# Optimization experiments

Measured on AMD Instinct MI355X. Metric: run time of the kernel, lower is better.

The kernel has to match this reference:

```python
import jax, jax.numpy as jnp
import numpy as np

B, C, H, W = 32, 384, 56, 56
SPARSE = 8
HEADS = 8
HIDDEN = 4 * C
EPS = 1e-5


def _ln(x, g, b):
    m = jnp.mean(x, axis=-1, keepdims=True)
    v = jnp.mean((x - m) ** 2, axis=-1, keepdims=True)
    return (x - m) * jax.lax.rsqrt(v + EPS) * g + b


def setup_inputs() -> dict:
    key = jax.random.key(0)
    ks = jax.random.split(key, 12)
    s = 0.02
    return {
        "x": jax.random.normal(ks[0], (B, C, H, W), jnp.float32),
        "ln1_g": jnp.ones((C,), jnp.float32),
        "ln1_b": jnp.zeros((C,), jnp.float32),
        "qkv_w": jax.random.normal(ks[1], (C, 3 * C), jnp.float32) * s,
        "proj_w": jax.random.normal(ks[2], (C, C), jnp.float32) * s,
        "proj_b": jnp.zeros((C,), jnp.float32),
        "ln2_g": jnp.ones((C,), jnp.float32),
        "ln2_b": jnp.zeros((C,), jnp.float32),
        "fc1_w": jax.random.normal(ks[3], (C, HIDDEN), jnp.float32) * s,
        "fc1_b": jnp.zeros((HIDDEN,), jnp.float32),
        "dw_w": jax.random.normal(ks[4], (HIDDEN, 1, 3, 3), jnp.float32) * np.sqrt(2.0 / 9.0),
        "dw_b": jnp.zeros((HIDDEN,), jnp.float32),
        "fc2_w": jax.random.normal(ks[5], (HIDDEN, C), jnp.float32) * s,
        "fc2_b": jnp.zeros((C,), jnp.float32),
        "gamma1": jnp.full((C,), 1e-6, jnp.float32),
        "gamma2": jnp.full((C,), 1e-6, jnp.float32),
    }


def reference(x, ln1_g, ln1_b, qkv_w, proj_w, proj_b, ln2_g, ln2_b,
              fc1_w, fc1_b, dw_w, dw_b, fc2_w, fc2_b, gamma1, gamma2):
    Bx, Cx, Hx, Wx = x.shape
    s = SPARSE
    g = Hx // s  # grid size; H divisible by sparse_size per module assert
    N = Hx * Wx
    hd = Cx // HEADS
    scale = hd ** (-0.5)

    x_before = x.reshape(Bx, Cx, N).transpose(0, 2, 1)  # [B,N,C]

    # alter_sparse: gather tokens spaced g apart into s x s windows
    xw = x.transpose(0, 2, 3, 1).reshape(Bx, s, g, s, g, Cx)
    xw = xw.transpose(0, 2, 4, 1, 3, 5).reshape(Bx * g * g, s * s, Cx)

    # attention on windows
    h = _ln(xw, ln1_g, ln1_b)
    qkv = (h @ qkv_w).reshape(Bx * g * g, s * s, 3, HEADS, hd)
    q, k, v = (qkv[:, :, i].transpose(0, 2, 1, 3) for i in range(3))  # [Bw,h,n,d]
    attn = jax.nn.softmax(jnp.einsum('bhqd,bhkd->bhqk', q, k) * scale, axis=-1)
    o = jnp.einsum('bhqk,bhkd->bhqd', attn, v).transpose(0, 2, 1, 3)
    o = o.reshape(Bx * g * g, s * s, Cx) @ proj_w + proj_b

    # alter_unsparse: scatter windows back to spatial layout
    o = o.reshape(Bx, g, g, s, s, Cx).transpose(0, 3, 1, 4, 2, 5)
    o = o.reshape(Bx, Hx, Wx, Cx).reshape(Bx, N, Cx)

    x1 = x_before + gamma1 * o

    # MLP with depthwise conv
    m = _ln(x1, ln2_g, ln2_b) @ fc1_w + fc1_b  # [B,N,hidden]
    m2 = m.transpose(0, 2, 1).reshape(Bx, HIDDEN, Hx, Wx)
    m2 = jax.lax.conv_general_dilated(
        m2, dw_w, window_strides=(1, 1), padding=((1, 1), (1, 1)),
        dimension_numbers=('NCHW', 'OIHW', 'NCHW'),
        feature_group_count=HIDDEN) + dw_b[None, :, None, None]
    m = m2.reshape(Bx, HIDDEN, N).transpose(0, 2, 1)
    m = jax.nn.gelu(m, approximate=False)
    m = m @ fc2_w + fc2_b

    x2 = x1 + gamma2 * m
    return x2.transpose(0, 2, 1).reshape(Bx, Cx, Hx, Wx)
```

## Files before the change

### kernel.cpp

```cpp
#include <hip/hip_runtime.h>
#include <hip/hip_bf16.h>

typedef __hip_bfloat16 bf16;
typedef float v4f __attribute__((ext_vector_type(4)));
typedef __attribute__((ext_vector_type(8))) short short8;

__device__ __forceinline__ float b2f(bf16 v) { return __bfloat162float(v); }
__device__ __forceinline__ bf16 f2b(float v) { return __float2bfloat16(v); }

__device__ __forceinline__ void gload_lds16(const bf16* g, bf16* l) {
    __builtin_amdgcn_global_load_lds((__attribute__((address_space(1))) void*)(void*)g,
                                     (__attribute__((address_space(3))) void*)l, 16, 0, 0);
}

#define BB 32
#define CD 384
#define HH 56
#define ND 3136
#define HID 1536
#define GG 7
#define SS 8
#define MROWS 100352

__device__ __forceinline__ int wrow_to_token(int orow) {
    int w = orow >> 6, t = orow & 63;
    int bb = w / 49, wr = w % 49;
    int gy = wr / GG, gx = wr % GG;
    int sy = t >> 3, sx = t & 7;
    return bb * ND + (sy * GG + gy) * HH + (sx * GG + gx);
}

__global__ __launch_bounds__(256) void transpose_f2b_k(const float* __restrict__ in,
                                                       bf16* __restrict__ out, int R, int Cc)
{
    __shared__ float tile[32][33];
    int c0 = blockIdx.x * 32, r0 = blockIdx.y * 32;
    size_t bb = blockIdx.z;
    int tx = threadIdx.x & 31, ty = threadIdx.x >> 5;
    const float* ip = in + bb * (size_t)R * Cc;
    bf16* op = out + bb * (size_t)R * Cc;
#pragma unroll
    for (int i = 0; i < 4; i++)
        tile[ty + i * 8][tx] = ip[(size_t)(r0 + ty + i * 8) * Cc + (c0 + tx)];
    __syncthreads();
#pragma unroll
    for (int i = 0; i < 4; i++)
        op[(size_t)(c0 + ty + i * 8) * R + (r0 + tx)] = f2b(tile[tx][ty + i * 8]);
}

__global__ __launch_bounds__(256) void ln_k(const bf16* __restrict__ in,
                                            const float* __restrict__ g,
                                            const float* __restrict__ b,
                                            bf16* __restrict__ out,
                                            int row0, int gather)
{
    int wave = threadIdx.x >> 6, lane = threadIdx.x & 63;
    int row = row0 + blockIdx.x * 4 + wave;
    int src = gather ? wrow_to_token(row) : row;
    const bf16* ip = in + (size_t)src * CD;
    float vals[6];
    float s = 0.f, s2 = 0.f;
#pragma unroll
    for (int i = 0; i < 6; i++) {
        float v = b2f(ip[lane + i * 64]);
        vals[i] = v; s += v; s2 += v * v;
    }
#pragma unroll
    for (int off = 32; off >= 1; off >>= 1) {
        s  += __shfl_xor(s, off);
        s2 += __shfl_xor(s2, off);
    }
    float mean = s * (1.f / CD);
    float var = s2 * (1.f / CD) - mean * mean;
    float rstd = rsqrtf(var + 1e-5f);
    bf16* op = out + (size_t)(row - row0) * CD;
#pragma unroll
    for (int i = 0; i < 6; i++) {
        int c = lane + i * 64;
        op[c] = f2b((vals[i] - mean) * rstd * g[c] + b[c]);
    }
}

__global__ __launch_bounds__(256) void gemm_bt(const bf16* __restrict__ A,
                                               const bf16* __restrict__ Bt,
                                               const float* __restrict__ bias,
                                               bf16* __restrict__ Cm,
                                               int M, int N, int K, int gx)
{
    __shared__ __align__(16) bf16 As[128][32];
    __shared__ __align__(16) bf16 Bs[128][32];
    const int nwg = gridDim.x;
    const int q = nwg >> 3, r = nwg & 7;
    const int xcd = blockIdx.x & 7, id8 = blockIdx.x >> 3;
    const int wgid = (xcd < r ? xcd * (q + 1) : r * (q + 1) + (xcd - r) * q) + id8;
    const int m0 = (wgid / gx) * 128, n0 = (wgid % gx) * 128;

    const int tid = threadIdx.x;
    const int lane = tid & 63, wave = tid >> 6;
    const int rb = (wave >> 1) * 64, cb = (wave & 1) * 64;
    const int lr = lane & 15, ko = (lane >> 4) * 8;
    const int srow = lane >> 2;
    const int scol = (lane & 3) * 8;

    v4f acc[4][4];
#pragma unroll
    for (int i = 0; i < 4; i++)
#pragma unroll
        for (int j = 0; j < 4; j++) acc[i][j] = (v4f)0.f;

    for (int kk = 0; kk < K; kk += 32) {
        const int r0 = wave * 32;
#pragma unroll
        for (int h = 0; h < 2; h++) {
            int row = r0 + h * 16 + srow;
            gload_lds16(&A [(size_t)(m0 + row) * K + kk + scol], &As[r0 + h * 16][0]);
            gload_lds16(&Bt[(size_t)(n0 + row) * K + kk + scol], &Bs[r0 + h * 16][0]);
        }
        __syncthreads();
        short8 af[4], bfr[4];
#pragma unroll
        for (int mi = 0; mi < 4; mi++) af[mi]  = *(const short8*)&As[rb + mi * 16 + lr][ko];
#pragma unroll
        for (int ni = 0; ni < 4; ni++) bfr[ni] = *(const short8*)&Bs[cb + ni * 16 + lr][ko];
#pragma unroll
        for (int mi = 0; mi < 4; mi++)
#pragma unroll
            for (int ni = 0; ni < 4; ni++)
                acc[mi][ni] = __builtin_amdgcn_mfma_f32_16x16x32_bf16(af[mi], bfr[ni], acc[mi][ni], 0, 0, 0);
        __syncthreads();
    }
#pragma unroll
    for (int ni = 0; ni < 4; ni++) {
        int col = n0 + cb + ni * 16 + lr;
        float bv = bias ? bias[col] : 0.f;
#pragma unroll
        for (int mi = 0; mi < 4; mi++) {
            int rowb = m0 + rb + mi * 16 + (lane >> 4) * 4;
#pragma unroll
            for (int r = 0; r < 4; r++)
                Cm[(size_t)(rowb + r) * N + col] = f2b(acc[mi][ni][r] + bv);
        }
    }
}

__global__ __launch_bounds__(64) void attn_mfma_k(const bf16* __restrict__ qkv,
                                                  bf16* __restrict__ o)
{
    __shared__ __align__(16) char lds[14336];
    char* Ps = lds;
    bf16* Vs = (bf16*)(lds + 8192);

    const int lane = threadIdx.x;
    const int lr = lane & 15, grp = lane >> 4;
    const int lw = blockIdx.x >> 3, head = blockIdx.x & 7;

    const bf16* base = qkv + (size_t)lw * 64 * 1152 + head * 48;

#pragma unroll
    for (int it = 0; it < 6; it++) {
        int i = it * 64 + lane;
        int t = i / 6, s = i - t * 6;
        *(uint4*)((char*)Vs + t * 96 + s * 16) =
            *(const uint4*)(base + (size_t)t * 1152 + 768 + s * 8);
    }

    v4f accs[4][4];
#pragma unroll
    for (int mi = 0; mi < 4; mi++)
#pragma unroll
        for (int ni = 0; ni < 4; ni++) accs[mi][ni] = (v4f)0.f;

    const short8 z8 = (short8)0;
    {
        short8 qf[4], kf[4];
#pragma unroll
        for (int mi = 0; mi < 4; mi++)
            qf[mi] = *(const short8*)(base + (size_t)(mi * 16 + lr) * 1152 + grp * 8);
#pragma unroll
        for (int ni = 0; ni < 4; ni++)
            kf[ni] = *(const short8*)(base + 384 + (size_t)(ni * 16 + lr) * 1152 + grp * 8);
#pragma unroll
        for (int mi = 0; mi < 4; mi++)
#pragma unroll
            for (int ni = 0; ni < 4; ni++)
                accs[mi][ni] = __builtin_amdgcn_mfma_f32_16x16x32_bf16(qf[mi], kf[ni], accs[mi][ni], 0, 0, 0);
#pragma unroll
        for (int mi = 0; mi < 4; mi++)
            qf[mi] = (grp < 2) ? *(const short8*)(base + (size_t)(mi * 16 + lr) * 1152 + 32 + grp * 8) : z8;
#pragma unroll
        for (int ni = 0; ni < 4; ni++)
            kf[ni] = (grp < 2) ? *(const short8*)(base + 384 + (size_t)(ni * 16 + lr) * 1152 + 32 + grp * 8) : z8;
#pragma unroll
        for (int mi = 0; mi < 4; mi++)
#pragma unroll
            for (int ni = 0; ni < 4; ni++)
                accs[mi][ni] = __builtin_amdgcn_mfma_f32_16x16x32_bf16(qf[mi], kf[ni], accs[mi][ni], 0, 0, 0);
    }

    const float scale = 0.14433756729740643f;
#pragma unroll
    for (int mi = 0; mi < 4; mi++)
#pragma unroll
        for (int ni = 0; ni < 4; ni++) accs[mi][ni] *= scale;

    float inv_s[4][4];
#pragma unroll
    for (int mi = 0; mi < 4; mi++) {
#pragma unroll
        for (int r = 0; r < 4; r++) {
            float mx = fmaxf(fmaxf(accs[mi][0][r], accs[mi][1][r]),
                             fmaxf(accs[mi][2][r], accs[mi][3][r]));
#pragma unroll
            for (int off = 8; off >= 1; off >>= 1) mx = fmaxf(mx, __shfl_xor(mx, off));
            float sum = 0.f;
#pragma unroll
            for (int ni = 0; ni < 4; ni++) {
                float e = __expf(accs[mi][ni][r] - mx);
                accs[mi][ni][r] = e;
                sum += e;
            }
#pragma unroll
            for (int off = 8; off >= 1; off >>= 1) sum += __shfl_xor(sum, off);
            inv_s[mi][r] = 1.f / sum;
        }
    }

#pragma unroll
    for (int mi = 0; mi < 4; mi++)
#pragma unroll
        for (int ni = 0; ni < 4; ni++)
#pragma unroll
            for (int r = 0; r < 4; r++) {
                int i = mi * 16 + grp * 4 + r;
                int j = ni * 16 + lr;
                int byte = (i * 128 + j * 2) ^ ((i & 7) << 4);
                *(bf16*)(Ps + byte) = f2b(accs[mi][ni][r]);
            }

    v4f acco[4][3];
#pragma unroll
    for (int mi = 0; mi < 4; mi++)
#pragma unroll
        for (int ni = 0; ni < 3; ni++) acco[mi][ni] = (v4f)0.f;

    const short* vsp = (const short*)Vs;
#pragma unroll
    for (int kk = 0; kk < 2; kk++) {
        int k0 = kk * 32 + grp * 8;
        short8 pf[4];
#pragma unroll
        for (int mi = 0; mi < 4; mi++) {
            int row = mi * 16 + lr;
            int byte = (row * 128 + k0 * 2) ^ ((row & 7) << 4);
            pf[mi] = *(const short8*)(Ps + byte);
        }
        short8 vf[3];
#pragma unroll
        for (int ni = 0; ni < 3; ni++) {
#pragma unroll
            for (int jj = 0; jj < 8; jj++)
                vf[ni][jj] = vsp[(k0 + jj) * 48 + ni * 16 + lr];
        }
#pragma unroll
        for (int mi = 0; mi < 4; mi++)
#pragma unroll
            for (int ni = 0; ni < 3; ni++)
                acco[mi][ni] = __builtin_amdgcn_mfma_f32_16x16x32_bf16(pf[mi], vf[ni], acco[mi][ni], 0, 0, 0);
    }

    bf16* op = o + (size_t)lw * 64 * CD + head * 48;
#pragma unroll
    for (int mi = 0; mi < 4; mi++)
#pragma unroll
        for (int r = 0; r < 4; r++) {
            int t = mi * 16 + grp * 4 + r;
            float is = inv_s[mi][r];
#pragma unroll
            for (int ni = 0; ni < 3; ni++)
                op[(size_t)t * CD + ni * 16 + lr] = f2b(acco[mi][ni][r] * is);
        }
}

__global__ __launch_bounds__(256) void resid1_k(const bf16* __restrict__ xt,
                                                const bf16* __restrict__ oprojc,
                                                const float* __restrict__ gamma1,
                                                bf16* __restrict__ x1, int row0)
{
    int idx = blockIdx.x * 256 + threadIdx.x;
    int lrow = idx / CD, c = idx % CD;
    int token = wrow_to_token(row0 + lrow);
    size_t xi = (size_t)token * CD + c;
    x1[xi] = f2b(b2f(xt[xi]) + gamma1[c] * b2f(oprojc[idx]));
}

__global__ __launch_bounds__(256) void dwconv_gelu_k(const bf16* __restrict__ m1c,
                                                     const float* __restrict__ wgt,
                                                     const float* __restrict__ bias,
                                                     bf16* __restrict__ gc)
{
    const int c  = blockIdx.x * 64 + (threadIdx.x & 63);
    const int xq = threadIdx.x >> 6;
    const int xx = blockIdx.y * 8 + xq * 2;
    const int lb = blockIdx.z >> 2;
    const int ys = (blockIdx.z & 3) * 14;

    float w9[9];
#pragma unroll
    for (int i = 0; i < 9; i++) w9[i] = wgt[c * 9 + i];
    const float bs = bias[c];

    const bf16* base = m1c + (size_t)lb * ND * HID + c;
    bool  v[4];
    const bf16* colp[4];
#pragma unroll
    for (int i = 0; i < 4; i++) {
        int xc = xx - 1 + i;
        v[i] = (xc >= 0 && xc < HH);
        int xcl = xc < 0 ? 0 : (xc > HH - 1 ? HH - 1 : xc);
        colp[i] = base + (size_t)xcl * HID;
    }
    const size_t ystride = (size_t)HH * HID;

    float win[3][4];
    {
        int ym = ys - 1;
        int ymc = ym < 0 ? 0 : ym;
        bool yv = (ym >= 0);
#pragma unroll
        for (int i = 0; i < 4; i++)
            win[0][i] = (yv && v[i]) ? b2f(colp[i][(size_t)ymc * ystride]) : 0.f;
#pragma unroll
        for (int i = 0; i < 4; i++)
            win[1][i] = v[i] ? b2f(colp[i][(size_t)ys * ystride]) : 0.f;
    }

#pragma unroll
    for (int s = 0; s < 14; s++) {
        const int y = ys + s;
        const int yp = y + 1;
        const bool yv = (yp < HH);
        const int ypc = yv ? yp : (HH - 1);
#pragma unroll
        for (int i = 0; i < 4; i++)
            win[2][i] = (yv && v[i]) ? b2f(colp[i][(size_t)ypc * ystride]) : 0.f;

        float a0 = bs, a1 = bs;
#pragma unroll
        for (int r = 0; r < 3; r++)
#pragma unroll
            for (int j = 0; j < 3; j++) {
                a0 = fmaf(w9[r * 3 + j], win[r][j],     a0);
                a1 = fmaf(w9[r * 3 + j], win[r][j + 1], a1);
            }
        float g0 = 0.5f * a0 * (1.f + erff(a0 * 0.70710678118654752f));
        float g1 = 0.5f * a1 * (1.f + erff(a1 * 0.70710678118654752f));
        size_t o0 = ((size_t)lb * ND + (size_t)y * HH + xx) * HID + c;
        gc[o0]       = f2b(g0);
        gc[o0 + HID] = f2b(g1);

#pragma unroll
        for (int i = 0; i < 4; i++) { win[0][i] = win[1][i]; win[1][i] = win[2][i]; }
    }
}

__global__ __launch_bounds__(256) void resid2_k(const bf16* __restrict__ x1,
                                                const bf16* __restrict__ m2c,
                                                const float* __restrict__ gamma2,
                                                float* __restrict__ out, int b0)
{
    __shared__ float tile[32][33];
    int n0 = blockIdx.x * 32, c0 = blockIdx.y * 32;
    int lb = blockIdx.z, gb = b0 + lb;
    int tx = threadIdx.x & 31, ty = threadIdx.x >> 5;
#pragma unroll
    for (int i = 0; i < 4; i++) {
        int n = n0 + ty + i * 8, c = c0 + tx;
        size_t sx1 = ((size_t)gb * ND + n) * CD + c;
        size_t sm  = ((size_t)lb * ND + n) * CD + c;
        tile[ty + i * 8][tx] = b2f(x1[sx1]) + gamma2[c] * b2f(m2c[sm]);
    }
    __syncthreads();
#pragma unroll
    for (int i = 0; i < 4; i++) {
        int c = c0 + ty + i * 8, n = n0 + tx;
        out[((size_t)gb * CD + c) * ND + n] = tile[tx][ty + i * 8];
    }
}

extern "C" void kernel_launch(void* const* d_in, const int* in_sizes, int n_in,
                              void* d_out, int out_size, void* d_ws, size_t ws_size,
                              hipStream_t stream) {
    const float* x      = (const float*)d_in[0];
    const float* ln1_g  = (const float*)d_in[1];
    const float* ln1_b  = (const float*)d_in[2];
    const float* qkv_w  = (const float*)d_in[3];
    const float* proj_w = (const float*)d_in[4];
    const float* proj_b = (const float*)d_in[5];
    const float* ln2_g  = (const float*)d_in[6];
    const float* ln2_b  = (const float*)d_in[7];
    const float* fc1_w  = (const float*)d_in[8];
    const float* fc1_b  = (const float*)d_in[9];
    const float* dw_w   = (const float*)d_in[10];
    const float* dw_b   = (const float*)d_in[11];
    const float* fc2_w  = (const float*)d_in[12];
    const float* fc2_b  = (const float*)d_in[13];
    const float* gamma1 = (const float*)d_in[14];
    const float* gamma2 = (const float*)d_in[15];
    float* out = (float*)d_out;

    const size_t SZ_TOK = (size_t)MROWS * CD * 2;
    const size_t S0 = 2 * SZ_TOK;
    const size_t WTS = 3538944;

    const size_t attn_end8 = S0 + (size_t)(MROWS / 8) * CD * 2 + (size_t)(MROWS / 8) * 1152 * 2;
    int cm = 16;
    {
        size_t mc2 = (size_t)(BB / 8) * ND;
        size_t mlp_end8 = S0 + mc2 * CD * 2 + 2 * mc2 * HID * 2;
        size_t tot8 = (mlp_end8 > attn_end8 ? mlp_end8 : attn_end8) + WTS;
        if (ws_size >= tot8) cm = 8;
    }
    const int nb = BB / cm;
    const int Mc2 = nb * ND;
    const size_t sz_h2 = (size_t)Mc2 * CD * 2;
    const size_t sz_m1 = (size_t)Mc2 * HID * 2;
    const size_t mlp_end = S0 + sz_h2 + 2 * sz_m1;

    int ca = 0;
    size_t sz_h = 0, sz_qk = 0, attn_end = 0;
    for (int cand = 2; cand <= 8 && !ca; cand <<= 1) {
        int McA_ = MROWS / cand;
        size_t h_ = (size_t)McA_ * CD * 2, qk_ = (size_t)McA_ * 1152 * 2;
        size_t ae = S0 + h_ + qk_;
        size_t tot = (mlp_end > ae ? mlp_end : ae) + WTS;
        if (ws_size >= tot) { ca = cand; sz_h = h_; sz_qk = qk_; attn_end = ae; }
    }
    if (!ca) return;
    const int McA = MROWS / ca;

    const size_t Wo = (mlp_end > attn_end ? mlp_end : attn_end);

    char* w = (char*)d_ws;
    bf16* xt      = (bf16*)(w + 0);
    bf16* x1      = (bf16*)(w + SZ_TOK);
    bf16* hc      = (bf16*)(w + S0);
    bf16* qkvc    = (bf16*)(w + S0 + sz_h);
    bf16* h2c     = (bf16*)(w + S0);
    bf16* m1c     = (bf16*)(w + S0 + sz_h2);
    bf16* gc      = (bf16*)(w + S0 + sz_h2 + sz_m1);
    bf16* qkv_wt  = (bf16*)(w + Wo);
    bf16* proj_wt = (bf16*)(w + Wo + 884736);
    bf16* fc1_wt  = (bf16*)(w + Wo + 884736 + 294912);
    bf16* fc2_wt  = (bf16*)(w + Wo + 884736 + 294912 + 1179648);

    dim3 blk(256);

    transpose_f2b_k<<<dim3(98, 12, 32), blk, 0, stream>>>(x, xt, CD, ND);
    transpose_f2b_k<<<dim3(36, 12, 1), blk, 0, stream>>>(qkv_w, qkv_wt, CD, 1152);
    transpose_f2b_k<<<dim3(12, 12, 1), blk, 0, stream>>>(proj_w, proj_wt, CD, CD);
    transpose_f2b_k<<<dim3(48, 12, 1), blk, 0, stream>>>(fc1_w, fc1_wt, CD, HID);
    transpose_f2b_k<<<dim3(12, 48, 1), blk, 0, stream>>>(fc2_w, fc2_wt, HID, CD);

    for (int ch = 0; ch < ca; ch++) {
        int row0 = ch * McA;
        ln_k<<<McA / 4, blk, 0, stream>>>(xt, ln1_g, ln1_b, hc, row0, 1);
        gemm_bt<<<dim3(9 * (McA / 128)), blk, 0, stream>>>(hc, qkv_wt, nullptr, qkvc, McA, 1152, CD, 9);
        attn_mfma_k<<<(McA / 64) * 8, dim3(64), 0, stream>>>(qkvc, hc);
        gemm_bt<<<dim3(3 * (McA / 128)), blk, 0, stream>>>(hc, proj_wt, proj_b, qkvc, McA, CD, CD, 3);
        resid1_k<<<(McA * CD) / 256, blk, 0, stream>>>(xt, qkvc, gamma1, x1, row0);
    }

    for (int ch = 0; ch < cm; ch++) {
        int r0 = ch * Mc2, b0 = ch * nb;
        ln_k<<<Mc2 / 4, blk, 0, stream>>>(x1, ln2_g, ln2_b, h2c, r0, 0);
        gemm_bt<<<dim3(12 * (Mc2 / 128)), blk, 0, stream>>>(h2c, fc1_wt, fc1_b, m1c, Mc2, HID, CD, 12);
        dwconv_gelu_k<<<dim3(HID / 64, 7, nb * 4), blk, 0, stream>>>(m1c, dw_w, dw_b, gc);
        gemm_bt<<<dim3(3 * (Mc2 / 128)), blk, 0, stream>>>(gc, fc2_wt, fc2_b, h2c, Mc2, CD, HID, 3);
        resid2_k<<<dim3(98, 12, nb), blk, 0, stream>>>(x1, h2c, gamma2, out, b0);
    }
}
```

Baseline: 1.784 ms.

## Double-buffer GEMM LDS tiles and fuse residual-1 into proj GEMM epilogue

The GEMM now keeps two LDS buffers and issues the next K-tile's global-to-LDS loads before computing on the current one, using explicit vmcnt waits and barriers so load latency overlaps the MFMA work. The proj GEMM epilogue also applies gamma1, the window-to-token unscatter and the residual add directly. This removes the separate resid1 kernel and its round trip of the projection output through memory. The cost is doubled LDS per block, which may reduce occupancy, and scattered uncoalesced stores in the fused epilogue.

```diff
diff --git a/kernel.cpp b/kernel.cpp
--- a/kernel.cpp
+++ b/kernel.cpp
@@ -85,10 +85,13 @@
                                                const bf16* __restrict__ Bt,
                                                const float* __restrict__ bias,
                                                bf16* __restrict__ Cm,
-                                               int M, int N, int K, int gx)
+                                               int M, int N, int K, int gx,
+                                               const bf16* __restrict__ xt,
+                                               const float* __restrict__ g1,
+                                               int row0)
 {
-    __shared__ __align__(16) bf16 As[128][32];
-    __shared__ __align__(16) bf16 Bs[128][32];
+    __shared__ __align__(16) bf16 As[2][128][32];
+    __shared__ __align__(16) bf16 Bs[2][128][32];
     const int nwg = gridDim.x;
     const int q = nwg >> 3, r = nwg & 7;
     const int xcd = blockIdx.x & 7, id8 = blockIdx.x >> 3;
@@ -99,36 +102,56 @@
     const int lane = tid & 63, wave = tid >> 6;
     const int rb = (wave >> 1) * 64, cb = (wave & 1) * 64;
     const int lr = lane & 15, ko = (lane >> 4) * 8;
+    const int r0s = wave * 32;
     const int srow = lane >> 2;
     const int scol = (lane & 3) * 8;
 
+    auto STAGE = [&](int bi, int kk0) {
+#pragma unroll
+        for (int h = 0; h < 2; h++) {
+            int row = r0s + h * 16 + srow;
+            gload_lds16(&A [(size_t)(m0 + row) * K + kk0 + scol], &As[bi][r0s + h * 16][0]);
+            gload_lds16(&Bt[(size_t)(n0 + row) * K + kk0 + scol], &Bs[bi][r0s + h * 16][0]);
+        }
+    };
+
     v4f acc[4][4];
 #pragma unroll
     for (int i = 0; i < 4; i++)
 #pragma unroll
         for (int j = 0; j < 4; j++) acc[i][j] = (v4f)0.f;
 
-    for (int kk = 0; kk < K; kk += 32) {
-        const int r0 = wave * 32;
-#pragma unroll
-        for (int h = 0; h < 2; h++) {
-            int row = r0 + h * 16 + srow;
-            gload_lds16(&A [(size_t)(m0 + row) * K + kk + scol], &As[r0 + h * 16][0]);
-            gload_lds16(&Bt[(size_t)(n0 + row) * K + kk + scol], &Bs[r0 + h * 16][0]);
-        }
-        __syncthreads();
+    const int nt = K >> 5;
+    int cur = 0;
+    STAGE(0, 0);
+
+    for (int t = 0; t < nt; t++) {
+        if (t + 1 < nt) {
+            STAGE(cur ^ 1, (t + 1) << 5);
+            asm volatile("s_waitcnt vmcnt(4)" ::: "memory");
+        } else {
+            asm volatile("s_waitcnt vmcnt(0)" ::: "memory");
+        }
+        __builtin_amdgcn_s_barrier();
+        __builtin_amdgcn_sched_barrier(0);
+
         short8 af[4], bfr[4];
 #pragma unroll
-        for (int mi = 0; mi < 4; mi++) af[mi]  = *(const short8*)&As[rb + mi * 16 + lr][ko];
-#pragma unroll
-        for (int ni = 0; ni < 4; ni++) bfr[ni] = *(const short8*)&Bs[cb + ni * 16 + lr][ko];
+        for (int mi = 0; mi < 4; mi++) af[mi]  = *(const short8*)&As[cur][rb + mi * 16 + lr][ko];
+#pragma unroll
+        for (int ni = 0; ni < 4; ni++) bfr[ni] = *(const short8*)&Bs[cur][cb + ni * 16 + lr][ko];
 #pragma unroll
         for (int mi = 0; mi < 4; mi++)
 #pragma unroll
             for (int ni = 0; ni < 4; ni++)
                 acc[mi][ni] = __builtin_amdgcn_mfma_f32_16x16x32_bf16(af[mi], bfr[ni], acc[mi][ni], 0, 0, 0);
-        __syncthreads();
-    }
+
+        asm volatile("s_waitcnt lgkmcnt(0)" ::: "memory");
+        __builtin_amdgcn_sched_barrier(0);
+        __builtin_amdgcn_s_barrier();
+        cur ^= 1;
+    }
+
 #pragma unroll
     for (int ni = 0; ni < 4; ni++) {
         int col = n0 + cb + ni * 16 + lr;
@@ -136,9 +159,19 @@
 #pragma unroll
         for (int mi = 0; mi < 4; mi++) {
             int rowb = m0 + rb + mi * 16 + (lane >> 4) * 4;
-#pragma unroll
-            for (int r = 0; r < 4; r++)
-                Cm[(size_t)(rowb + r) * N + col] = f2b(acc[mi][ni][r] + bv);
+            if (g1 == nullptr) {
+#pragma unroll
+                for (int r2 = 0; r2 < 4; r2++)
+                    Cm[(size_t)(rowb + r2) * N + col] = f2b(acc[mi][ni][r2] + bv);
+            } else {
+                float gv = g1[col];
+#pragma unroll
+                for (int r2 = 0; r2 < 4; r2++) {
+                    int token = wrow_to_token(row0 + rowb + r2);
+                    size_t xi = (size_t)token * CD + col;
+                    Cm[xi] = f2b(b2f(xt[xi]) + gv * (acc[mi][ni][r2] + bv));
+                }
+            }
         }
     }
 }
@@ -279,18 +312,6 @@
             for (int ni = 0; ni < 3; ni++)
                 op[(size_t)t * CD + ni * 16 + lr] = f2b(acco[mi][ni][r] * is);
         }
-}
-
-__global__ __launch_bounds__(256) void resid1_k(const bf16* __restrict__ xt,
-                                                const bf16* __restrict__ oprojc,
-                                                const float* __restrict__ gamma1,
-                                                bf16* __restrict__ x1, int row0)
-{
-    int idx = blockIdx.x * 256 + threadIdx.x;
-    int lrow = idx / CD, c = idx % CD;
-    int token = wrow_to_token(row0 + lrow);
-    size_t xi = (size_t)token * CD + c;
-    x1[xi] = f2b(b2f(xt[xi]) + gamma1[c] * b2f(oprojc[idx]));
 }
 
 __global__ __launch_bounds__(256) void dwconv_gelu_k(const bf16* __restrict__ m1c,
@@ -464,18 +485,21 @@
     for (int ch = 0; ch < ca; ch++) {
         int row0 = ch * McA;
         ln_k<<<McA / 4, blk, 0, stream>>>(xt, ln1_g, ln1_b, hc, row0, 1);
-        gemm_bt<<<dim3(9 * (McA / 128)), blk, 0, stream>>>(hc, qkv_wt, nullptr, qkvc, McA, 1152, CD, 9);
+        gemm_bt<<<dim3(9 * (McA / 128)), blk, 0, stream>>>(hc, qkv_wt, nullptr, qkvc,
+                                                           McA, 1152, CD, 9, nullptr, nullptr, 0);
         attn_mfma_k<<<(McA / 64) * 8, dim3(64), 0, stream>>>(qkvc, hc);
-        gemm_bt<<<dim3(3 * (McA / 128)), blk, 0, stream>>>(hc, proj_wt, proj_b, qkvc, McA, CD, CD, 3);
-        resid1_k<<<(McA * CD) / 256, blk, 0, stream>>>(xt, qkvc, gamma1, x1, row0);
+        gemm_bt<<<dim3(3 * (McA / 128)), blk, 0, stream>>>(hc, proj_wt, proj_b, x1,
+                                                           McA, CD, CD, 3, xt, gamma1, row0);
     }
 
     for (int ch = 0; ch < cm; ch++) {
         int r0 = ch * Mc2, b0 = ch * nb;
         ln_k<<<Mc2 / 4, blk, 0, stream>>>(x1, ln2_g, ln2_b, h2c, r0, 0);
-        gemm_bt<<<dim3(12 * (Mc2 / 128)), blk, 0, stream>>>(h2c, fc1_wt, fc1_b, m1c, Mc2, HID, CD, 12);
+        gemm_bt<<<dim3(12 * (Mc2 / 128)), blk, 0, stream>>>(h2c, fc1_wt, fc1_b, m1c,
+                                                            Mc2, HID, CD, 12, nullptr, nullptr, 0);
         dwconv_gelu_k<<<dim3(HID / 64, 7, nb * 4), blk, 0, stream>>>(m1c, dw_w, dw_b, gc);
-        gemm_bt<<<dim3(3 * (Mc2 / 128)), blk, 0, stream>>>(gc, fc2_wt, fc2_b, h2c, Mc2, CD, HID, 3);
+        gemm_bt<<<dim3(3 * (Mc2 / 128)), blk, 0, stream>>>(gc, fc2_wt, fc2_b, h2c,
+                                                           Mc2, CD, HID, 3, nullptr, nullptr, 0);
         resid2_k<<<dim3(98, 12, nb), blk, 0, stream>>>(x1, h2c, gamma2, out, b0);
     }
 }
```

Result: no change. 1.817 ms (+1.8%).
